# Kernel optimization log

Measured on AMD Instinct MI355X. Metric: run time of the kernel, lower is better.

## Reference

```python
import jax, jax.numpy as jnp
import numpy as np

EPS = 1e-8


def setup_inputs() -> dict:
    key = jax.random.key(0)
    ks = jax.random.split(key, 8)
    B, N, D = 8, 2048, 768
    H, R = 768, 4
    return {
        "x": jax.random.normal(ks[0], (B, N, D), dtype=jnp.float32),
        "scale": jnp.ones((D,), dtype=jnp.float32),
        "U": jax.random.normal(ks[1], (H, R), dtype=jnp.float32) * 0.02,
        "V": jax.random.normal(ks[2], (H, R), dtype=jnp.float32) * 0.02,
        "S_param": jax.random.normal(ks[3], (H, H), dtype=jnp.float32) * 0.01,
        "Bm": jax.random.normal(ks[4], (H, D), dtype=jnp.float32) * (1.0 / np.sqrt(D)),
        "Cm": jax.random.normal(ks[5], (D, H), dtype=jnp.float32) * (1.0 / np.sqrt(H)),
        "gate_w": jax.random.normal(ks[6], (D, D), dtype=jnp.float32) * (1.0 / np.sqrt(D)),
        "gate_b": jnp.zeros((D,), dtype=jnp.float32),
        "alpha": jnp.full((1,), 0.1, dtype=jnp.float32),
    }


def reference(x, scale, U, V, S_param, Bm, Cm, gate_w, gate_b, alpha):
    B, N, D = x.shape
    H = Bm.shape[0]
    # A = diag(A_diag) + U V^T + (S - S^T); A_diag is a fixed buffer.
    A_diag = -jnp.linspace(1.0, float(H), H, dtype=x.dtype) / H
    A = jnp.diag(A_diag) + U @ V.T + (S_param - S_param.T)
    At = A.T  # apply as h @ A.T
    # RMSNorm
    rms = jnp.sqrt(jnp.mean(x * x, axis=-1, keepdims=True) + EPS)
    xn = x / rms * scale
    # Precompute input injections u_t = x_t @ B.T for all t: (N, B, H)
    u = jnp.einsum('bnd,hd->nbh', xn, Bm)

    def step(h, ut):
        h = h @ At + ut
        return h, h @ Cm.T  # (B, D)

    h0 = jnp.zeros((B, H), dtype=x.dtype)
    _, y_fwd = jax.lax.scan(step, h0, u)                 # (N, B, D)
    _, y_bwd = jax.lax.scan(step, h0, u, reverse=True)   # (N, B, D), indexed in time order
    y = 0.5 * (y_fwd + y_bwd)
    y = jnp.swapaxes(y, 0, 1)  # (B, N, D)
    # Gate
    g = jax.nn.sigmoid(jnp.einsum('bnd,ed->bne', xn, gate_w) + gate_b)
    y = y * g
    # Skip (dropout is identity in eval)
    return x + alpha * y
```

## Files before the change

kernel.cpp:

```cpp
#include <hip/hip_runtime.h>


typedef short  bfrag __attribute__((ext_vector_type(8)));
typedef float  ffrag __attribute__((ext_vector_type(4)));
typedef float  f4    __attribute__((ext_vector_type(4)));
typedef short  s4v   __attribute__((ext_vector_type(4)));

#define DEV static __device__ __forceinline__
#define Hn 768
#define FLS 132
#define BLS 260

DEV unsigned short f2bf(float f) {
  unsigned u = __float_as_uint(f);
  u += 0x7fffu + ((u >> 16) & 1u);
  return (unsigned short)(u >> 16);
}
DEV float bf2f(unsigned short s) { return __uint_as_float(((unsigned)s) << 16); }

DEV ffrag mfma16(bfrag a, bfrag b, ffrag c) {
  return __builtin_amdgcn_mfma_f32_16x16x32_bf16(a, b, c, 0, 0, 0);
}

DEV void glds16(const unsigned short* g, unsigned short* l) {
  __builtin_amdgcn_global_load_lds(
      (const __attribute__((address_space(1))) unsigned int*)g,
      (__attribute__((address_space(3))) unsigned int*)l, 16, 0, 0);
}

union BF8 { bfrag v; unsigned short u[8]; };

__global__ __launch_bounds__(256) void k_abuild(
    const float* __restrict__ U, const float* __restrict__ V,
    const float* __restrict__ S, const float* __restrict__ Bm,
    const float* __restrict__ Cm, const float* __restrict__ gw,
    float* __restrict__ Af, float* __restrict__ AfT,
    unsigned short* __restrict__ Abf,
    unsigned short* __restrict__ Bmb, unsigned short* __restrict__ Cmb,
    unsigned short* __restrict__ gwb, unsigned short* __restrict__ zp) {
  int i = blockIdx.x;
  int task = blockIdx.y;
  if (task == 0) {
    float u0 = U[i*4+0], u1 = U[i*4+1], u2 = U[i*4+2], u3 = U[i*4+3];
    for (int j = threadIdx.x; j < Hn; j += 256) {
      float a = u0*V[j*4+0] + u1*V[j*4+1] + u2*V[j*4+2] + u3*V[j*4+3]
              + S[i*Hn+j] - S[j*Hn+i];
      if (i == j) a += -(float)(i+1) / 768.0f;
      Af[i*Hn+j]  = a;
      AfT[j*Hn+i] = a;
      Abf[i*Hn+j] = f2bf(a);
    }
    if (i == 0) for (int j = threadIdx.x; j < 1024; j += 256) zp[j] = 0;
  } else {
    const float* src = (task==1) ? Bm : (task==2) ? Cm : gw;
    unsigned short* dst = (task==1) ? Bmb : (task==2) ? Cmb : gwb;
    for (int j = threadIdx.x; j < Hn; j += 256) dst[i*Hn+j] = f2bf(src[i*Hn+j]);
  }
}

__global__ __launch_bounds__(256) void k_rms(
    const float* __restrict__ x, const float* __restrict__ scale,
    unsigned short* __restrict__ xn) {
  int row  = blockIdx.x * 4 + (threadIdx.x >> 6);
  int lane = threadIdx.x & 63;
  int b = row >> 11, t = row & 2047;
  const float* xr = x + (long)row * Hn;
  float v[12];
  float ss = 0.f;
#pragma unroll
  for (int j = 0; j < 12; ++j) { v[j] = xr[lane + j*64]; ss += v[j]*v[j]; }
#pragma unroll
  for (int off = 1; off < 64; off <<= 1) ss += __shfl_xor(ss, off);
  float inv = 1.0f / sqrtf(ss / 768.0f + 1e-8f);
  unsigned short* dst = xn + ((long)t * 8 + b) * Hn;
#pragma unroll
  for (int j = 0; j < 12; ++j) dst[lane + j*64] = f2bf(v[j] * inv * scale[lane + j*64]);
}

__global__ __launch_bounds__(512) void k_sq(
    const float* __restrict__ X, const float* __restrict__ XT,
    float* __restrict__ Z, float* __restrict__ ZT,
    unsigned short* __restrict__ Zbf) {
  int tid = threadIdx.x, lane = tid & 63, w = tid >> 6;
  int mw = w >> 2, nw = w & 3, l15 = lane & 15, lhi = lane >> 4;
  int rb = blockIdx.x * 64, cb = blockIdx.y * 128;
  ffrag acc[2][2] = {};
  for (int kt = 0; kt < 24; ++kt) {
    int k0 = kt*32 + lhi*8;
    BF8 ah[2], al[2], bh[2], bl[2];
#pragma unroll
    for (int mt = 0; mt < 2; ++mt) {
      const f4* p = (const f4*)(X + (long)(rb + mw*32 + mt*16 + l15) * Hn + k0);
      f4 x0 = p[0], x1 = p[1];
#pragma unroll
      for (int j = 0; j < 8; ++j) {
        float f = (j < 4) ? x0[j] : x1[j-4];
        unsigned short h = f2bf(f);
        ah[mt].u[j] = h; al[mt].u[j] = f2bf(f - bf2f(h));
      }
    }
#pragma unroll
    for (int nt = 0; nt < 2; ++nt) {
      const f4* p = (const f4*)(XT + (long)(cb + nw*32 + nt*16 + l15) * Hn + k0);
      f4 x0 = p[0], x1 = p[1];
#pragma unroll
      for (int j = 0; j < 8; ++j) {
        float f = (j < 4) ? x0[j] : x1[j-4];
        unsigned short h = f2bf(f);
        bh[nt].u[j] = h; bl[nt].u[j] = f2bf(f - bf2f(h));
      }
    }
#pragma unroll
    for (int mt = 0; mt < 2; ++mt)
#pragma unroll
      for (int nt = 0; nt < 2; ++nt) {
        acc[mt][nt] = mfma16(ah[mt].v, bh[nt].v, acc[mt][nt]);
        acc[mt][nt] = mfma16(ah[mt].v, bl[nt].v, acc[mt][nt]);
        acc[mt][nt] = mfma16(al[mt].v, bh[nt].v, acc[mt][nt]);
      }
  }
#pragma unroll
  for (int mt = 0; mt < 2; ++mt)
#pragma unroll
    for (int nt = 0; nt < 2; ++nt)
#pragma unroll
      for (int q = 0; q < 4; ++q) {
        int grow = rb + mw*32 + mt*16 + lhi*4 + q;
        int gcol = cb + nw*32 + nt*16 + l15;
        float vv = acc[mt][nt][q];
        Z[(long)grow*Hn + gcol] = vv;
        ZT[(long)gcol*Hn + grow] = vv;
        Zbf[(long)grow*Hn + gcol] = f2bf(vv);
      }
}

template<int MODE>
__global__ __launch_bounds__(512) void k_lvl(
    const unsigned short* __restrict__ A0s, const unsigned short* __restrict__ B0s,
    const unsigned short* __restrict__ res, unsigned short* __restrict__ outb,
    const unsigned short* __restrict__ zp, int sh) {
  constexpr int NS   = (MODE == 2) ? 2 : 1;
  constexpr int BUFS = NS * 4096 + 8192;
  __shared__ __align__(16) unsigned short ldsb[2 * BUFS];

  const int tid = threadIdx.x, lane = tid & 63, w = tid >> 6;
  const int l15 = lane & 15, lhi = lane >> 4;
  const int wr = w >> 2, wc = w & 3;

  const int nwg = gridDim.x;
  const int q8 = nwg >> 3, r8 = nwg & 7, xcd = blockIdx.x & 7, fo = blockIdx.x >> 3;
  const int wg = (xcd < r8 ? xcd*(q8+1) : r8*(q8+1) + (xcd - r8)*q8) + fo;
  const int cb = wg % 3, rbk = wg / 3;
  const long r0  = (long)rbk * 128;
  const long bc0 = (long)cb * 256;
  const int dir = (MODE == 1 && r0 >= 16384) ? 1 : 0;

  bool skip = false;
  if (MODE == 1)
    skip = dir ? (r0 >= 32768 - sh) : (r0 + 128 <= sh);

  const int rowin = lane >> 2, ch = lane & 3;
  const int rA = w*16 + rowin;
  const int cswz = ch ^ ((rowin ^ (rowin >> 2)) & 3);
  long gA[NS]; bool vA[NS];
#pragma unroll
  for (int s = 0; s < NS; ++s) {
    long gr; bool ok = true;
    if (MODE == 0) {
      gr = r0 + rA;
    } else if (MODE == 1) {
      gr = r0 + rA + (dir ? sh : -sh);
      ok = dir ? (gr < 32768) : (gr >= 0);
    } else {
      if (s == 0) { gr = r0 + rA - sh;         ok = (gr >= 0);    }
      else        { gr = r0 + rA + 16384 + sh; ok = (gr < 32768); }
    }
    vA[s] = ok; gA[s] = gr * Hn + cswz*8;
  }
  long gB[2];
#pragma unroll
  for (int j = 0; j < 2; ++j)
    gB[j] = (bc0 + j*128 + rA) * Hn + cswz*8;

  auto stage = [&](int buf, int kt) {
    const int ko = kt * 32;
    unsigned short* dst = ldsb + buf * BUFS;
#pragma unroll
    for (int s = 0; s < NS; ++s) {
      const unsigned short* g = vA[s] ? (A0s + gA[s] + ko) : zp;
      glds16(g, dst + s*4096 + w*512);
    }
#pragma unroll
    for (int j = 0; j < 2; ++j)
      glds16(B0s + gB[j] + ko, dst + NS*4096 + j*4096 + w*512);
  };

  ffrag acc[4][4] = {};
  const int cx = (lhi ^ ((l15 ^ (l15 >> 2)) & 3)) * 8;

  if (!skip) {
    stage(0, 0);
    __syncthreads();
    int cur = 0;
    for (int kt = 0; kt < 24; ++kt) {
      if (kt < 23) stage(cur ^ 1, kt + 1);
      const unsigned short* L = ldsb + cur * BUFS;
      bfrag a[NS][4], b[4];
#pragma unroll
      for (int mt = 0; mt < 4; ++mt) {
        const int row = wr*64 + mt*16 + l15;
#pragma unroll
        for (int s = 0; s < NS; ++s)
          a[s][mt] = *(const bfrag*)&L[s*4096 + row*32 + cx];
      }
#pragma unroll
      for (int nt = 0; nt < 4; ++nt) {
        const int row = wc*64 + nt*16 + l15;
        b[nt] = *(const bfrag*)&L[NS*4096 + row*32 + cx];
      }
#pragma unroll
      for (int mt = 0; mt < 4; ++mt)
#pragma unroll
        for (int nt = 0; nt < 4; ++nt) {
          acc[mt][nt] = mfma16(a[0][mt], b[nt], acc[mt][nt]);
          if (NS == 2) acc[mt][nt] = mfma16(a[1][mt], b[nt], acc[mt][nt]);
        }
      __syncthreads();
      cur ^= 1;
    }
  }

  float* fl = (float*)ldsb;
#pragma unroll
  for (int p = 0; p < 4; ++p) {
    __syncthreads();
#pragma unroll
    for (int nt = 0; nt < 4; ++nt)
#pragma unroll
      for (int q = 0; q < 4; ++q)
        fl[(wr*16 + lhi*4 + q)*BLS + wc*64 + nt*16 + l15] = acc[p][nt][q];
    __syncthreads();
    for (int i = tid; i < 2048; i += 512) {
      const int srow = i >> 6;
      const int cc   = (i & 63) << 2;
      f4 v = *(const f4*)&fl[srow*BLS + cc];
      const long grow = r0 + (srow >> 4)*64 + p*16 + (srow & 15);
      const long gcol = bc0 + cc;
      const long go = grow * Hn + gcol;
      if (MODE == 0) {
        s4v ov;
#pragma unroll
        for (int j = 0; j < 4; ++j) ((unsigned short*)&ov)[j] = f2bf(v[j]);
        *(s4v*)&outb[go] = ov;
        *(s4v*)&outb[go + (long)16384*Hn] = ov;
      } else if (MODE == 1) {
        s4v rv = *(const s4v*)&res[go];
#pragma unroll
        for (int j = 0; j < 4; ++j) v[j] += bf2f(((unsigned short*)&rv)[j]);
        s4v ov;
#pragma unroll
        for (int j = 0; j < 4; ++j) ((unsigned short*)&ov)[j] = f2bf(v[j]);
        *(s4v*)&outb[go] = ov;
      } else {
        s4v ra = *(const s4v*)&res[go];
        s4v rb2 = *(const s4v*)&res[go + (long)16384*Hn];
#pragma unroll
        for (int j = 0; j < 4; ++j)
          v[j] += bf2f(((unsigned short*)&ra)[j]) + bf2f(((unsigned short*)&rb2)[j]);
        s4v ov;
#pragma unroll
        for (int j = 0; j < 4; ++j) ((unsigned short*)&ov)[j] = f2bf(v[j]);
        *(s4v*)&outb[go] = ov;
      }
    }
  }
}

__global__ __launch_bounds__(256) void k_fin(
    const unsigned short* __restrict__ A0s, const unsigned short* __restrict__ A1s,
    const unsigned short* __restrict__ B0s, const unsigned short* __restrict__ B1s,
    const unsigned short* __restrict__ zp,
    const float* __restrict__ gb, const float* __restrict__ alpha,
    const float* __restrict__ x, float* __restrict__ outf) {
  __shared__ __align__(16) char smem[2 * 4 * 8192];
  unsigned short* ldsb = (unsigned short*)smem;

  const int tid = threadIdx.x, lane = tid & 63, w = tid >> 6;
  const int l15 = lane & 15, lhi = lane >> 4;
  const int wr = w >> 1, wc = w & 1;

  const int nwg = gridDim.x;
  const int q8 = nwg >> 3, r8 = nwg & 7, xcd = blockIdx.x & 7, fo = blockIdx.x >> 3;
  const int wg = (xcd < r8 ? xcd*(q8+1) : r8*(q8+1) + (xcd - r8)*q8) + fo;
  const int cb = wg % 6, rbk = wg / 6;
  const long r0 = (long)rbk * 128;
  const long bc0 = (long)cb * 128;

  const int rowin = lane >> 2, ch = lane & 3;
  long gA[2][2]; long gB[2][2]; int lbase[2];
#pragma unroll
  for (int jj = 0; jj < 2; ++jj) {
    const int inst = w*2 + jj;
    const int r = inst*16 + rowin;
    const int c = ch ^ ((r ^ (r >> 2)) & 3);
    lbase[jj] = inst * 512;
    gA[0][jj] = (r0 + r) * Hn + c*8;
    gA[1][jj] = gA[0][jj];
    gB[0][jj] = (bc0 + r) * Hn + c*8;
    gB[1][jj] = gB[0][jj];
  }

  auto stage = [&](int buf, int kt) {
    const int ko = kt * 32;
    unsigned short* dst = ldsb + buf * 16384;
#pragma unroll
    for (int jj = 0; jj < 2; ++jj) {
      glds16(A0s + gA[0][jj] + ko, dst + 0*4096 + lbase[jj]);
      glds16(A1s + gA[1][jj] + ko, dst + 1*4096 + lbase[jj]);
      glds16(B0s + gB[0][jj] + ko, dst + 2*4096 + lbase[jj]);
      glds16(B1s + gB[1][jj] + ko, dst + 3*4096 + lbase[jj]);
    }
  };

  ffrag acc[4][4] = {};
  ffrag accZ[4][4] = {};
  const int cx = (lhi ^ ((l15 ^ (l15 >> 2)) & 3)) * 8;

  stage(0, 0);
  int cur = 0;
  for (int kt = 0; kt < 24; ++kt) {
    asm volatile("s_waitcnt vmcnt(0)" ::: "memory");
    __builtin_amdgcn_s_barrier();
    if (kt < 23) stage(cur ^ 1, kt + 1);
    const unsigned short* L = ldsb + cur * 16384;
    bfrag a[2][4], b0[4], b1[4];
#pragma unroll
    for (int mt = 0; mt < 4; ++mt) {
      const int row = wr*64 + mt*16 + l15;
      a[0][mt] = *(const bfrag*)&L[row*32 + cx];
      a[1][mt] = *(const bfrag*)&L[4096 + row*32 + cx];
    }
#pragma unroll
    for (int nt = 0; nt < 4; ++nt) {
      const int row = wc*64 + nt*16 + l15;
      b0[nt] = *(const bfrag*)&L[2*4096 + row*32 + cx];
      b1[nt] = *(const bfrag*)&L[3*4096 + row*32 + cx];
    }
#pragma unroll
    for (int mt = 0; mt < 4; ++mt)
#pragma unroll
      for (int nt = 0; nt < 4; ++nt) {
        acc[mt][nt]  = mfma16(a[0][mt], b0[nt], acc[mt][nt]);
        accZ[mt][nt] = mfma16(a[1][mt], b1[nt], accZ[mt][nt]);
      }
    cur ^= 1;
  }

  const float al = alpha[0];
  float gvals[4];
#pragma unroll
  for (int nt = 0; nt < 4; ++nt) gvals[nt] = gb[bc0 + wc*64 + nt*16 + l15];
#pragma unroll
  for (int mt = 0; mt < 4; ++mt)
#pragma unroll
    for (int nt = 0; nt < 4; ++nt)
#pragma unroll
      for (int q = 0; q < 4; ++q) {
        float z = accZ[mt][nt][q] + gvals[nt];
        float g = 1.0f / (1.0f + __expf(-z));
        acc[mt][nt][q] *= al * 0.5f * g;
      }

  float* fl = (float*)smem;
#pragma unroll
  for (int hh = 0; hh < 2; ++hh) {
    __syncthreads();
    if (wr == hh) {
#pragma unroll
      for (int mt = 0; mt < 4; ++mt)
#pragma unroll
        for (int nt = 0; nt < 4; ++nt)
#pragma unroll
          for (int q = 0; q < 4; ++q)
            fl[(mt*16 + lhi*4 + q)*FLS + wc*64 + nt*16 + l15] = acc[mt][nt][q];
    }
    __syncthreads();
    for (int i = tid; i < 2048; i += 256) {
      const int row = i >> 5;
      const int cc  = (i & 31) << 2;
      f4 v = *(const f4*)&fl[row*FLS + cc];
      const long grow = r0 + hh*64 + row;
      const long gcol = bc0 + cc;
      const long t = grow >> 3, b = grow & 7;
      const long o = (b*2048 + t)*Hn + gcol;
      f4 xv = *(const f4*)&x[o];
      f4 ov;
#pragma unroll
      for (int j = 0; j < 4; ++j) ov[j] = xv[j] + v[j];
      *(f4*)&outf[o] = ov;
    }
  }
}

extern "C" void kernel_launch(void* const* d_in, const int* in_sizes, int n_in,
                              void* d_out, int out_size, void* d_ws, size_t ws_size,
                              hipStream_t stream) {
  const float* x     = (const float*)d_in[0];
  const float* scale = (const float*)d_in[1];
  const float* U     = (const float*)d_in[2];
  const float* V     = (const float*)d_in[3];
  const float* S     = (const float*)d_in[4];
  const float* Bm    = (const float*)d_in[5];
  const float* Cm    = (const float*)d_in[6];
  const float* gw    = (const float*)d_in[7];
  const float* gb    = (const float*)d_in[8];
  const float* alpha = (const float*)d_in[9];
  float* out = (float*)d_out;

  char* p = (char*)d_ws;
  auto alloc = [&](size_t sz) { char* r = p; p += (sz + 255) & ~(size_t)255; return r; };

  const size_t SZ_X  = (size_t)32768 * Hn * sizeof(unsigned short);
  const size_t SZ_BF = (size_t)16384 * Hn * sizeof(unsigned short);
  const size_t SZ_M  = (size_t)Hn * Hn * sizeof(float);
  const size_t SZ_MB = (size_t)Hn * Hn * sizeof(unsigned short);

  unsigned short* xn = (unsigned short*)alloc(SZ_BF);
  unsigned short* XA = (unsigned short*)alloc(SZ_X);
  unsigned short* XB = (unsigned short*)alloc(SZ_X);
  float* Af  = (float*)alloc(SZ_M);
  float* AfT = (float*)alloc(SZ_M);
  float* P1  = (float*)alloc(SZ_M);
  float* P1T = (float*)alloc(SZ_M);
  float* P2  = (float*)alloc(SZ_M);
  float* P2T = (float*)alloc(SZ_M);
  unsigned short* Abf = (unsigned short*)alloc(SZ_MB);
  unsigned short* Ab[10];
  for (int i = 0; i < 10; ++i) Ab[i] = (unsigned short*)alloc(SZ_MB);
  unsigned short* Bmb = (unsigned short*)alloc(SZ_MB);
  unsigned short* Cmb = (unsigned short*)alloc(SZ_MB);
  unsigned short* gwb = (unsigned short*)alloc(SZ_MB);
  unsigned short* zp  = (unsigned short*)alloc(1024 * sizeof(unsigned short));

  if ((size_t)(p - (char*)d_ws) > ws_size) return;

  k_abuild<<<dim3(768, 4), 256, 0, stream>>>(U, V, S, Bm, Cm, gw,
      Af, AfT, Abf, Bmb, Cmb, gwb, zp);
  k_rms<<<4096, 256, 0, stream>>>(x, scale, xn);

  const float* sx = Af; const float* sxt = AfT;
  float* za = P1; float* zat = P1T; float* zb = P2; float* zbt = P2T;
  for (int i = 0; i < 10; ++i) {
    k_sq<<<dim3(12, 6), 512, 0, stream>>>(sx, sxt, za, zat, Ab[i]);
    sx = za; sxt = zat;
    float* t1 = za; float* t2 = zat; za = zb; zat = zbt; zb = t1; zbt = t2;
  }

  k_lvl<0><<<384, 512, 0, stream>>>(xn, Bmb, nullptr, XA, zp, 0);

  unsigned short* src = XA; unsigned short* dst = XB;
  for (int i = 0; i < 10; ++i) {
    const unsigned short* W = (i == 0) ? Abf : Ab[i-1];
    k_lvl<1><<<768, 512, 0, stream>>>(src, W, src, dst, zp, 8 << i);
    unsigned short* t = src; src = dst; dst = t;
  }
  k_lvl<2><<<384, 512, 0, stream>>>(src, Ab[9], src, XB, zp, 8192);

  k_fin<<<768, 256, 0, stream>>>(XB, xn, Cmb, gwb, zp, gb, alpha, x, out);
}
```

Measured before the change: 1.241 ms.

## Enlarge scan-level GEMM tiles, triple-buffer loads, move gate GEMM into input-projection kernel

The scan-level kernel now uses 256x256 tiles with a three-stage LDS ring buffer and vmcnt-based waits, in place of 128x256 double-buffered tiles. This halves the workgroup count and raises reuse of each staged tile. The gate GEMM is moved out of the final kernel into a new fused input kernel that computes u = xn·Bᵀ and z = xn·gate_wᵀ together, sharing the xn tile and storing z in bf16. The final kernel then runs a single GEMM and applies the sigmoid in its epilogue. The cost is higher register and LDS pressure, an extra bf16 z buffer read and write, and lower occupancy.

New measurement: 1.375 ms. 1.11x slower.

```diff
diff --git a/kernel.cpp b/kernel.cpp
--- a/kernel.cpp
+++ b/kernel.cpp
@@ -26,6 +26,11 @@
   __builtin_amdgcn_global_load_lds(
       (const __attribute__((address_space(1))) unsigned int*)g,
       (__attribute__((address_space(3))) unsigned int*)l, 16, 0, 0);
+}
+
+template<int N> DEV void vwait() {
+  if constexpr (N == 0)      asm volatile("s_waitcnt vmcnt(0)" ::: "memory");
+  else if constexpr (N == 4) asm volatile("s_waitcnt vmcnt(4)" ::: "memory");
 }
 
 union BF8 { bfrag v; unsigned short u[8]; };
@@ -134,13 +139,112 @@
       }
 }
 
-template<int MODE>
-__global__ __launch_bounds__(512) void k_lvl(
+__global__ __launch_bounds__(512) void k_lvl256(
     const unsigned short* __restrict__ A0s, const unsigned short* __restrict__ B0s,
     const unsigned short* __restrict__ res, unsigned short* __restrict__ outb,
     const unsigned short* __restrict__ zp, int sh) {
-  constexpr int NS   = (MODE == 2) ? 2 : 1;
-  constexpr int BUFS = NS * 4096 + 8192;
+  __shared__ __align__(16) unsigned short ldsb[3 * 16384];
+
+  const int tid = threadIdx.x, lane = tid & 63, w = tid >> 6;
+  const int l15 = lane & 15, lhi = lane >> 4;
+  const int wr = w >> 2, wc = w & 3;
+
+  const int nwg = gridDim.x;
+  const int q8 = nwg >> 3, r8 = nwg & 7, xcd = blockIdx.x & 7, fo = blockIdx.x >> 3;
+  const int wg = (xcd < r8 ? xcd*(q8+1) : r8*(q8+1) + (xcd - r8)*q8) + fo;
+  const int cb = wg % 3, rbk = wg / 3;
+  const long r0  = (long)rbk * 256;
+  const long bc0 = (long)cb * 256;
+  const int dir = (r0 >= 16384) ? 1 : 0;
+
+  const bool skip = dir ? (r0 >= 32768 - sh) : (r0 + 256 <= sh);
+
+  const int rowin = lane >> 2, ch = lane & 3;
+  long gA[2]; bool vA[2]; long gB[2]; int lbase[2];
+#pragma unroll
+  for (int j = 0; j < 2; ++j) {
+    const int rl = j*128 + w*16 + rowin;
+    const int c = ch ^ ((rl ^ (rl >> 2)) & 3);
+    lbase[j] = j*4096 + w*512;
+    long gr = r0 + rl + (dir ? sh : -sh);
+    vA[j] = dir ? (gr < 32768) : (gr >= 0);
+    gA[j] = gr * Hn + c*8;
+    gB[j] = (bc0 + rl) * Hn + c*8;
+  }
+
+  auto stage = [&](int buf, int kt) {
+    const int ko = kt * 32;
+    unsigned short* dst = ldsb + buf * 16384;
+#pragma unroll
+    for (int j = 0; j < 2; ++j) {
+      const unsigned short* g = vA[j] ? (A0s + gA[j] + ko) : zp;
+      glds16(g, dst + lbase[j]);
+      glds16(B0s + gB[j] + ko, dst + 8192 + lbase[j]);
+    }
+  };
+
+  ffrag acc[8][4] = {};
+  const int cx = (lhi ^ ((l15 ^ (l15 >> 2)) & 3)) * 8;
+
+  if (!skip) {
+    stage(0, 0); stage(1, 1);
+    for (int kt = 0; kt < 24; ++kt) {
+      if (kt < 23) vwait<4>(); else vwait<0>();
+      __builtin_amdgcn_s_barrier();
+      if (kt + 2 <= 23) stage((kt + 2) % 3, kt + 2);
+      const unsigned short* L = ldsb + (kt % 3) * 16384;
+      bfrag b[4];
+#pragma unroll
+      for (int nt = 0; nt < 4; ++nt)
+        b[nt] = *(const bfrag*)&L[8192 + (wc*64 + nt*16 + l15)*32 + cx];
+#pragma unroll
+      for (int mh = 0; mh < 2; ++mh) {
+        bfrag a[4];
+#pragma unroll
+        for (int m4 = 0; m4 < 4; ++m4)
+          a[m4] = *(const bfrag*)&L[(wr*128 + (mh*4 + m4)*16 + l15)*32 + cx];
+#pragma unroll
+        for (int m4 = 0; m4 < 4; ++m4)
+#pragma unroll
+          for (int nt = 0; nt < 4; ++nt)
+            acc[mh*4 + m4][nt] = mfma16(a[m4], b[nt], acc[mh*4 + m4][nt]);
+      }
+    }
+  }
+
+  float* fl = (float*)ldsb;
+#pragma unroll
+  for (int p = 0; p < 8; ++p) {
+    __syncthreads();
+#pragma unroll
+    for (int nt = 0; nt < 4; ++nt)
+#pragma unroll
+      for (int q = 0; q < 4; ++q)
+        fl[(wr*16 + lhi*4 + q)*BLS + wc*64 + nt*16 + l15] = acc[p][nt][q];
+    __syncthreads();
+    for (int i = tid; i < 2048; i += 512) {
+      const int srow = i >> 6;
+      const int cc   = (i & 63) << 2;
+      f4 v = *(const f4*)&fl[srow*BLS + cc];
+      const long grow = r0 + (srow >> 4)*128 + p*16 + (srow & 15);
+      const long gcol = bc0 + cc;
+      const long go = grow * Hn + gcol;
+      s4v rv = *(const s4v*)&res[go];
+#pragma unroll
+      for (int j = 0; j < 4; ++j) v[j] += bf2f(((unsigned short*)&rv)[j]);
+      s4v ov;
+#pragma unroll
+      for (int j = 0; j < 4; ++j) ((unsigned short*)&ov)[j] = f2bf(v[j]);
+      *(s4v*)&outb[go] = ov;
+    }
+  }
+}
+
+__global__ __launch_bounds__(512) void k_cmb(
+    const unsigned short* __restrict__ A0s, const unsigned short* __restrict__ B0s,
+    const unsigned short* __restrict__ res, unsigned short* __restrict__ outb,
+    const unsigned short* __restrict__ zp, int sh) {
+  constexpr int BUFS = 2 * 4096 + 8192;
   __shared__ __align__(16) unsigned short ldsb[2 * BUFS];
 
   const int tid = threadIdx.x, lane = tid & 63, w = tid >> 6;
@@ -153,30 +257,13 @@
   const int cb = wg % 3, rbk = wg / 3;
   const long r0  = (long)rbk * 128;
   const long bc0 = (long)cb * 256;
-  const int dir = (MODE == 1 && r0 >= 16384) ? 1 : 0;
-
-  bool skip = false;
-  if (MODE == 1)
-    skip = dir ? (r0 >= 32768 - sh) : (r0 + 128 <= sh);
 
   const int rowin = lane >> 2, ch = lane & 3;
   const int rA = w*16 + rowin;
   const int cswz = ch ^ ((rowin ^ (rowin >> 2)) & 3);
-  long gA[NS]; bool vA[NS];
-#pragma unroll
-  for (int s = 0; s < NS; ++s) {
-    long gr; bool ok = true;
-    if (MODE == 0) {
-      gr = r0 + rA;
-    } else if (MODE == 1) {
-      gr = r0 + rA + (dir ? sh : -sh);
-      ok = dir ? (gr < 32768) : (gr >= 0);
-    } else {
-      if (s == 0) { gr = r0 + rA - sh;         ok = (gr >= 0);    }
-      else        { gr = r0 + rA + 16384 + sh; ok = (gr < 32768); }
-    }
-    vA[s] = ok; gA[s] = gr * Hn + cswz*8;
-  }
+  long gA[2]; bool vA[2];
+  { long g0 = r0 + rA - sh;         vA[0] = (g0 >= 0);    gA[0] = g0 * Hn + cswz*8; }
+  { long g1 = r0 + rA + 16384 + sh; vA[1] = (g1 < 32768); gA[1] = g1 * Hn + cswz*8; }
   long gB[2];
 #pragma unroll
   for (int j = 0; j < 2; ++j)
@@ -186,48 +273,45 @@
     const int ko = kt * 32;
     unsigned short* dst = ldsb + buf * BUFS;
 #pragma unroll
-    for (int s = 0; s < NS; ++s) {
+    for (int s = 0; s < 2; ++s) {
       const unsigned short* g = vA[s] ? (A0s + gA[s] + ko) : zp;
       glds16(g, dst + s*4096 + w*512);
     }
 #pragma unroll
     for (int j = 0; j < 2; ++j)
-      glds16(B0s + gB[j] + ko, dst + NS*4096 + j*4096 + w*512);
+      glds16(B0s + gB[j] + ko, dst + 2*4096 + j*4096 + w*512);
   };
 
   ffrag acc[4][4] = {};
   const int cx = (lhi ^ ((l15 ^ (l15 >> 2)) & 3)) * 8;
 
-  if (!skip) {
-    stage(0, 0);
-    __syncthreads();
-    int cur = 0;
-    for (int kt = 0; kt < 24; ++kt) {
-      if (kt < 23) stage(cur ^ 1, kt + 1);
-      const unsigned short* L = ldsb + cur * BUFS;
-      bfrag a[NS][4], b[4];
-#pragma unroll
-      for (int mt = 0; mt < 4; ++mt) {
-        const int row = wr*64 + mt*16 + l15;
-#pragma unroll
-        for (int s = 0; s < NS; ++s)
-          a[s][mt] = *(const bfrag*)&L[s*4096 + row*32 + cx];
-      }
+  stage(0, 0);
+  __syncthreads();
+  int cur = 0;
+  for (int kt = 0; kt < 24; ++kt) {
+    if (kt < 23) stage(cur ^ 1, kt + 1);
+    const unsigned short* L = ldsb + cur * BUFS;
+    bfrag a[2][4], b[4];
+#pragma unroll
+    for (int mt = 0; mt < 4; ++mt) {
+      const int row = wr*64 + mt*16 + l15;
+      a[0][mt] = *(const bfrag*)&L[row*32 + cx];
+      a[1][mt] = *(const bfrag*)&L[4096 + row*32 + cx];
+    }
+#pragma unroll
+    for (int nt = 0; nt < 4; ++nt) {
+      const int row = wc*64 + nt*16 + l15;
+      b[nt] = *(const bfrag*)&L[2*4096 + row*32 + cx];
+    }
+#pragma unroll
+    for (int mt = 0; mt < 4; ++mt)
 #pragma unroll
       for (int nt = 0; nt < 4; ++nt) {
-        const int row = wc*64 + nt*16 + l15;
-        b[nt] = *(const bfrag*)&L[NS*4096 + row*32 + cx];
-      }
-#pragma unroll
-      for (int mt = 0; mt < 4; ++mt)
-#pragma unroll
-        for (int nt = 0; nt < 4; ++nt) {
-          acc[mt][nt] = mfma16(a[0][mt], b[nt], acc[mt][nt]);
-          if (NS == 2) acc[mt][nt] = mfma16(a[1][mt], b[nt], acc[mt][nt]);
-        }
-      __syncthreads();
-      cur ^= 1;
-    }
+        acc[mt][nt] = mfma16(a[0][mt], b[nt], acc[mt][nt]);
+        acc[mt][nt] = mfma16(a[1][mt], b[nt], acc[mt][nt]);
+      }
+    __syncthreads();
+    cur ^= 1;
   }
 
   float* fl = (float*)ldsb;
@@ -247,43 +331,24 @@
       const long grow = r0 + (srow >> 4)*64 + p*16 + (srow & 15);
       const long gcol = bc0 + cc;
       const long go = grow * Hn + gcol;
-      if (MODE == 0) {
-        s4v ov;
-#pragma unroll
-        for (int j = 0; j < 4; ++j) ((unsigned short*)&ov)[j] = f2bf(v[j]);
-        *(s4v*)&outb[go] = ov;
-        *(s4v*)&outb[go + (long)16384*Hn] = ov;
-      } else if (MODE == 1) {
-        s4v rv = *(const s4v*)&res[go];
-#pragma unroll
-        for (int j = 0; j < 4; ++j) v[j] += bf2f(((unsigned short*)&rv)[j]);
-        s4v ov;
-#pragma unroll
-        for (int j = 0; j < 4; ++j) ((unsigned short*)&ov)[j] = f2bf(v[j]);
-        *(s4v*)&outb[go] = ov;
-      } else {
-        s4v ra = *(const s4v*)&res[go];
-        s4v rb2 = *(const s4v*)&res[go + (long)16384*Hn];
-#pragma unroll
-        for (int j = 0; j < 4; ++j)
-          v[j] += bf2f(((unsigned short*)&ra)[j]) + bf2f(((unsigned short*)&rb2)[j]);
-        s4v ov;
-#pragma unroll
-        for (int j = 0; j < 4; ++j) ((unsigned short*)&ov)[j] = f2bf(v[j]);
-        *(s4v*)&outb[go] = ov;
-      }
-    }
-  }
-}
-
-__global__ __launch_bounds__(256) void k_fin(
-    const unsigned short* __restrict__ A0s, const unsigned short* __restrict__ A1s,
-    const unsigned short* __restrict__ B0s, const unsigned short* __restrict__ B1s,
-    const unsigned short* __restrict__ zp,
-    const float* __restrict__ gb, const float* __restrict__ alpha,
-    const float* __restrict__ x, float* __restrict__ outf) {
-  __shared__ __align__(16) char smem[2 * 4 * 8192];
-  unsigned short* ldsb = (unsigned short*)smem;
+      s4v ra = *(const s4v*)&res[go];
+      s4v rb2 = *(const s4v*)&res[go + (long)16384*Hn];
+#pragma unroll
+      for (int j = 0; j < 4; ++j)
+        v[j] += bf2f(((unsigned short*)&ra)[j]) + bf2f(((unsigned short*)&rb2)[j]);
+      s4v ov;
+#pragma unroll
+      for (int j = 0; j < 4; ++j) ((unsigned short*)&ov)[j] = f2bf(v[j]);
+      *(s4v*)&outb[go] = ov;
+    }
+  }
+}
+
+__global__ __launch_bounds__(256) void k_uz(
+    const unsigned short* __restrict__ xn, const unsigned short* __restrict__ Bmb,
+    const unsigned short* __restrict__ gwb,
+    unsigned short* __restrict__ u, unsigned short* __restrict__ z) {
+  __shared__ __align__(16) unsigned short ldsb[2 * 3 * 4096];
 
   const int tid = threadIdx.x, lane = tid & 63, w = tid >> 6;
   const int l15 = lane & 15, lhi = lane >> 4;
@@ -297,28 +362,25 @@
   const long bc0 = (long)cb * 128;
 
   const int rowin = lane >> 2, ch = lane & 3;
-  long gA[2][2]; long gB[2][2]; int lbase[2];
+  long gA[2]; long gB[2]; int lbase[2];
 #pragma unroll
   for (int jj = 0; jj < 2; ++jj) {
     const int inst = w*2 + jj;
     const int r = inst*16 + rowin;
     const int c = ch ^ ((r ^ (r >> 2)) & 3);
     lbase[jj] = inst * 512;
-    gA[0][jj] = (r0 + r) * Hn + c*8;
-    gA[1][jj] = gA[0][jj];
-    gB[0][jj] = (bc0 + r) * Hn + c*8;
-    gB[1][jj] = gB[0][jj];
+    gA[jj] = (r0 + r) * Hn + c*8;
+    gB[jj] = (bc0 + r) * Hn + c*8;
   }
 
   auto stage = [&](int buf, int kt) {
     const int ko = kt * 32;
-    unsigned short* dst = ldsb + buf * 16384;
+    unsigned short* dst = ldsb + buf * 12288;
 #pragma unroll
     for (int jj = 0; jj < 2; ++jj) {
-      glds16(A0s + gA[0][jj] + ko, dst + 0*4096 + lbase[jj]);
-      glds16(A1s + gA[1][jj] + ko, dst + 1*4096 + lbase[jj]);
-      glds16(B0s + gB[0][jj] + ko, dst + 2*4096 + lbase[jj]);
-      glds16(B1s + gB[1][jj] + ko, dst + 3*4096 + lbase[jj]);
+      glds16(xn  + gA[jj] + ko, dst + 0*4096 + lbase[jj]);
+      glds16(Bmb + gB[jj] + ko, dst + 1*4096 + lbase[jj]);
+      glds16(gwb + gB[jj] + ko, dst + 2*4096 + lbase[jj]);
     }
   };
 
@@ -327,50 +389,135 @@
   const int cx = (lhi ^ ((l15 ^ (l15 >> 2)) & 3)) * 8;
 
   stage(0, 0);
+  __syncthreads();
   int cur = 0;
   for (int kt = 0; kt < 24; ++kt) {
-    asm volatile("s_waitcnt vmcnt(0)" ::: "memory");
-    __builtin_amdgcn_s_barrier();
     if (kt < 23) stage(cur ^ 1, kt + 1);
-    const unsigned short* L = ldsb + cur * 16384;
-    bfrag a[2][4], b0[4], b1[4];
-#pragma unroll
-    for (int mt = 0; mt < 4; ++mt) {
-      const int row = wr*64 + mt*16 + l15;
-      a[0][mt] = *(const bfrag*)&L[row*32 + cx];
-      a[1][mt] = *(const bfrag*)&L[4096 + row*32 + cx];
-    }
+    const unsigned short* L = ldsb + cur * 12288;
+    bfrag a[4], b0[4], b1[4];
+#pragma unroll
+    for (int mt = 0; mt < 4; ++mt)
+      a[mt] = *(const bfrag*)&L[(wr*64 + mt*16 + l15)*32 + cx];
 #pragma unroll
     for (int nt = 0; nt < 4; ++nt) {
       const int row = wc*64 + nt*16 + l15;
-      b0[nt] = *(const bfrag*)&L[2*4096 + row*32 + cx];
-      b1[nt] = *(const bfrag*)&L[3*4096 + row*32 + cx];
+      b0[nt] = *(const bfrag*)&L[1*4096 + row*32 + cx];
+      b1[nt] = *(const bfrag*)&L[2*4096 + row*32 + cx];
     }
 #pragma unroll
     for (int mt = 0; mt < 4; ++mt)
 #pragma unroll
       for (int nt = 0; nt < 4; ++nt) {
-        acc[mt][nt]  = mfma16(a[0][mt], b0[nt], acc[mt][nt]);
-        accZ[mt][nt] = mfma16(a[1][mt], b1[nt], accZ[mt][nt]);
-      }
+        acc[mt][nt]  = mfma16(a[mt], b0[nt], acc[mt][nt]);
+        accZ[mt][nt] = mfma16(a[mt], b1[nt], accZ[mt][nt]);
+      }
+    __syncthreads();
     cur ^= 1;
   }
 
+  float* fl = (float*)ldsb;
+#pragma unroll
+  for (int which = 0; which < 2; ++which) {
+#pragma unroll
+    for (int hh = 0; hh < 2; ++hh) {
+      __syncthreads();
+      if (wr == hh) {
+#pragma unroll
+        for (int mt = 0; mt < 4; ++mt)
+#pragma unroll
+          for (int nt = 0; nt < 4; ++nt)
+#pragma unroll
+            for (int q = 0; q < 4; ++q)
+              fl[(mt*16 + lhi*4 + q)*FLS + wc*64 + nt*16 + l15] =
+                  which ? accZ[mt][nt][q] : acc[mt][nt][q];
+      }
+      __syncthreads();
+      for (int i = tid; i < 2048; i += 256) {
+        const int row = i >> 5;
+        const int cc  = (i & 31) << 2;
+        f4 v = *(const f4*)&fl[row*FLS + cc];
+        const long go = (r0 + hh*64 + row) * Hn + bc0 + cc;
+        s4v ov;
+#pragma unroll
+        for (int j = 0; j < 4; ++j) ((unsigned short*)&ov)[j] = f2bf(v[j]);
+        if (which == 0) {
+          *(s4v*)&u[go] = ov;
+          *(s4v*)&u[go + (long)16384*Hn] = ov;
+        } else {
+          *(s4v*)&z[go] = ov;
+        }
+      }
+    }
+  }
+}
+
+__global__ __launch_bounds__(256) void k_fin2(
+    const unsigned short* __restrict__ A0s, const unsigned short* __restrict__ B0s,
+    const unsigned short* __restrict__ z,
+    const float* __restrict__ gb, const float* __restrict__ alpha,
+    const float* __restrict__ x, float* __restrict__ outf) {
+  __shared__ __align__(16) char smem[34048];
+  unsigned short* ldsb = (unsigned short*)smem;
+
+  const int tid = threadIdx.x, lane = tid & 63, w = tid >> 6;
+  const int l15 = lane & 15, lhi = lane >> 4;
+  const int wr = w >> 1, wc = w & 1;
+
+  const int nwg = gridDim.x;
+  const int q8 = nwg >> 3, r8 = nwg & 7, xcd = blockIdx.x & 7, fo = blockIdx.x >> 3;
+  const int wg = (xcd < r8 ? xcd*(q8+1) : r8*(q8+1) + (xcd - r8)*q8) + fo;
+  const int cb = wg % 6, rbk = wg / 6;
+  const long r0 = (long)rbk * 128;
+  const long bc0 = (long)cb * 128;
+
+  const int rowin = lane >> 2, ch = lane & 3;
+  long gA[2]; long gB[2]; int lbase[2];
+#pragma unroll
+  for (int jj = 0; jj < 2; ++jj) {
+    const int inst = w*2 + jj;
+    const int r = inst*16 + rowin;
+    const int c = ch ^ ((r ^ (r >> 2)) & 3);
+    lbase[jj] = inst * 512;
+    gA[jj] = (r0 + r) * Hn + c*8;
+    gB[jj] = (bc0 + r) * Hn + c*8;
+  }
+
+  auto stage = [&](int buf, int kt) {
+    const int ko = kt * 32;
+    unsigned short* dst = ldsb + buf * 8192;
+#pragma unroll
+    for (int jj = 0; jj < 2; ++jj) {
+      glds16(A0s + gA[jj] + ko, dst + lbase[jj]);
+      glds16(B0s + gB[jj] + ko, dst + 4096 + lbase[jj]);
+    }
+  };
+
+  ffrag acc[4][4] = {};
+  const int cx = (lhi ^ ((l15 ^ (l15 >> 2)) & 3)) * 8;
+
+  stage(0, 0);
+  __syncthreads();
+  int cur = 0;
+  for (int kt = 0; kt < 24; ++kt) {
+    if (kt < 23) stage(cur ^ 1, kt + 1);
+    const unsigned short* L = ldsb + cur * 8192;
+    bfrag a[4], b[4];
+#pragma unroll
+    for (int mt = 0; mt < 4; ++mt)
+      a[mt] = *(const bfrag*)&L[(wr*64 + mt*16 + l15)*32 + cx];
+#pragma unroll
+    for (int nt = 0; nt < 4; ++nt)
+      b[nt] = *(const bfrag*)&L[4096 + (wc*64 + nt*16 + l15)*32 + cx];
+#pragma unroll
+    for (int mt = 0; mt < 4; ++mt)
+#pragma unroll
+      for (int nt = 0; nt < 4; ++nt)
+        acc[mt][nt] = mfma16(a[mt], b[nt], acc[mt][nt]);
+    __syncthreads();
+    cur ^= 1;
+  }
+
   const float al = alpha[0];
-  float gvals[4];
-#pragma unroll
-  for (int nt = 0; nt < 4; ++nt) gvals[nt] = gb[bc0 + wc*64 + nt*16 + l15];
-#pragma unroll
-  for (int mt = 0; mt < 4; ++mt)
-#pragma unroll
-    for (int nt = 0; nt < 4; ++nt)
-#pragma unroll
-      for (int q = 0; q < 4; ++q) {
-        float z = accZ[mt][nt][q] + gvals[nt];
-        float g = 1.0f / (1.0f + __expf(-z));
-        acc[mt][nt][q] *= al * 0.5f * g;
-      }
-
   float* fl = (float*)smem;
 #pragma unroll
   for (int hh = 0; hh < 2; ++hh) {
@@ -391,12 +538,19 @@
       f4 v = *(const f4*)&fl[row*FLS + cc];
       const long grow = r0 + hh*64 + row;
       const long gcol = bc0 + cc;
+      const long go = grow * Hn + gcol;
+      s4v zv = *(const s4v*)&z[go];
+      f4 gbv = *(const f4*)&gb[gcol];
       const long t = grow >> 3, b = grow & 7;
       const long o = (b*2048 + t)*Hn + gcol;
       f4 xv = *(const f4*)&x[o];
       f4 ov;
 #pragma unroll
-      for (int j = 0; j < 4; ++j) ov[j] = xv[j] + v[j];
+      for (int j = 0; j < 4; ++j) {
+        float zz = bf2f(((unsigned short*)&zv)[j]) + gbv[j];
+        float g = 1.0f / (1.0f + __expf(-zz));
+        ov[j] = xv[j] + al * 0.5f * v[j] * g;
+      }
       *(f4*)&outf[o] = ov;
     }
   }
@@ -425,7 +579,8 @@
   const size_t SZ_M  = (size_t)Hn * Hn * sizeof(float);
   const size_t SZ_MB = (size_t)Hn * Hn * sizeof(unsigned short);
 
-  unsigned short* xn = (unsigned short*)alloc(SZ_BF);
+  unsigned short* xn   = (unsigned short*)alloc(SZ_BF);
+  unsigned short* zbuf = (unsigned short*)alloc(SZ_BF);
   unsigned short* XA = (unsigned short*)alloc(SZ_X);
   unsigned short* XB = (unsigned short*)alloc(SZ_X);
   float* Af  = (float*)alloc(SZ_M);
@@ -456,15 +611,15 @@
     float* t1 = za; float* t2 = zat; za = zb; zat = zbt; zb = t1; zbt = t2;
   }
 
-  k_lvl<0><<<384, 512, 0, stream>>>(xn, Bmb, nullptr, XA, zp, 0);
+  k_uz<<<768, 256, 0, stream>>>(xn, Bmb, gwb, XA, zbuf);
 
   unsigned short* src = XA; unsigned short* dst = XB;
   for (int i = 0; i < 10; ++i) {
     const unsigned short* W = (i == 0) ? Abf : Ab[i-1];
-    k_lvl<1><<<768, 512, 0, stream>>>(src, W, src, dst, zp, 8 << i);
+    k_lvl256<<<384, 512, 0, stream>>>(src, W, src, dst, zp, 8 << i);
     unsigned short* t = src; src = dst; dst = t;
   }
-  k_lvl<2><<<384, 512, 0, stream>>>(src, Ab[9], src, XB, zp, 8192);
-
-  k_fin<<<768, 256, 0, stream>>>(XB, xn, Cmb, gwb, zp, gb, alpha, x, out);
-}
+  k_cmb<<<384, 512, 0, stream>>>(src, Ab[9], src, XB, zp, 8192);
+
+  k_fin2<<<768, 256, 0, stream>>>(XB, Cmb, zbuf, gb, alpha, x, out);
+}
```
